# Kernel optimization log

Measured on AMD Instinct MI355X. Metric: run time of the kernel, lower is better.

The kernel has to match this reference:

```python
import jax, jax.numpy as jnp
import numpy as np

B, S, H = 2, 2048, 1024
NH, HD = 16, 64  # num heads, head dim
EPS = 1e-12


def setup_inputs() -> dict:
    key = jax.random.key(0)
    ks = jax.random.split(key, 10)
    scale = 0.02
    return {
        "hidden_states": jax.random.normal(ks[0], (B, S, H), jnp.float32),
        "attention_mask": jnp.zeros((B, 1, 1, S), jnp.float32),
        "Wq": jax.random.normal(ks[1], (H, H), jnp.float32) * scale,
        "bq": jnp.zeros((H,), jnp.float32),
        "Wk": jax.random.normal(ks[2], (H, H), jnp.float32) * scale,
        "bk": jnp.zeros((H,), jnp.float32),
        "Wv": jax.random.normal(ks[3], (H, H), jnp.float32) * scale,
        "bv": jnp.zeros((H,), jnp.float32),
        "Wo": jax.random.normal(ks[4], (H, H), jnp.float32) * scale,
        "bo": jnp.zeros((H,), jnp.float32),
        "ln_gamma": jnp.ones((H,), jnp.float32),
        "ln_beta": jnp.zeros((H,), jnp.float32),
    }


def _split_heads(x):
    # [B,S,H] -> [B,NH,S,HD]
    b, s, _ = x.shape
    return x.reshape(b, s, NH, HD).transpose(0, 2, 1, 3)


def reference(hidden_states, attention_mask, Wq, bq, Wk, bk, Wv, bv, Wo, bo, ln_gamma, ln_beta):
    q = _split_heads(hidden_states @ Wq + bq)
    k = _split_heads(hidden_states @ Wk + bk)
    v = _split_heads(hidden_states @ Wv + bv)

    # unfused SDPA, as in source: matmul -> scale -> mask -> softmax -> matmul
    scores = jnp.einsum('bhqd,bhkd->bhqk', q, k) / jnp.sqrt(jnp.float32(HD))
    scores = scores + attention_mask
    probs = jax.nn.softmax(scores, axis=-1)  # dropout p=0 (eval)
    ctx = jnp.einsum('bhqk,bhkd->bhqd', probs, v)
    ctx = ctx.transpose(0, 2, 1, 3).reshape(hidden_states.shape)  # [B,S,H]

    # BaseBertSelfOutput: dense -> (dropout p=0) -> LayerNorm(residual)
    out = ctx @ Wo + bo
    res = out + hidden_states
    mu = jnp.mean(res, axis=-1, keepdims=True)
    var = jnp.mean(jnp.square(res - mu), axis=-1, keepdims=True)
    normed = (res - mu) * jax.lax.rsqrt(var + EPS)
    return normed * ln_gamma + ln_beta
```

## Files before the change

kernel.cpp:

```cpp
#include <hip/hip_runtime.h>
#include <hip/hip_bf16.h>

#define B_  2
#define S_  2048
#define H_  1024
#define NH_ 16
#define HD_ 64
#define EPSLN 1e-12f

typedef short bf16x8 __attribute__((ext_vector_type(8)));
typedef float f32x4  __attribute__((ext_vector_type(4)));

__device__ __forceinline__ float bf2f(ushort u) {
    union { unsigned int i; float f; } v; v.i = ((unsigned int)u) << 16; return v.f;
}
__device__ __forceinline__ ushort f2bf(float f) {
    union { float f; unsigned int i; } v; v.f = f;
    unsigned int r = v.i + 0x7FFFu + ((v.i >> 16) & 1u);
    return (ushort)(r >> 16);
}
__device__ __forceinline__ ushort f2bf_hw(float f) {
    __hip_bfloat16 h = __float2bfloat16(f);
    return *reinterpret_cast<ushort*>(&h);
}
__device__ __forceinline__ unsigned int pack_bf2(float a, float b) {
    return ((unsigned int)f2bf_hw(b) << 16) | (unsigned int)f2bf_hw(a);
}

__global__ __launch_bounds__(256) void cvt_f32_bf16(const float* __restrict__ in,
                                                    ushort* __restrict__ out, int n) {
    int i = (blockIdx.x * 256 + threadIdx.x) * 4;
    float4 v = *(const float4*)&in[i];
    ushort4 o = make_ushort4(f2bf(v.x), f2bf(v.y), f2bf(v.z), f2bf(v.w));
    *(ushort4*)&out[i] = o;
}

__global__ __launch_bounds__(256) void transpose_cvt(
        const float* __restrict__ W0, const float* __restrict__ W1,
        const float* __restrict__ W2, const float* __restrict__ W3,
        ushort* __restrict__ T0, ushort* __restrict__ T1,
        ushort* __restrict__ T2, ushort* __restrict__ T3) {
    const int z = blockIdx.z;
    const float* in = (z == 0) ? W0 : (z == 1) ? W1 : (z == 2) ? W2 : W3;
    ushort* out     = (z == 0) ? T0 : (z == 1) ? T1 : (z == 2) ? T2 : T3;

    __shared__ float tile[64][65];
    const int bx = blockIdx.x * 64, by = blockIdx.y * 64;
    const int t = threadIdx.x;
    #pragma unroll
    for (int i = 0; i < 16; i++) {
        int idx = t + i * 256;
        int r = idx >> 6, c = idx & 63;
        tile[r][c] = in[(by + r) * 1024 + bx + c];
    }
    __syncthreads();
    #pragma unroll
    for (int i = 0; i < 16; i++) {
        int idx = t + i * 256;
        int r = idx >> 6, c = idx & 63;
        out[(bx + r) * 1024 + by + c] = f2bf(tile[c][r]);
    }
}

__global__ __launch_bounds__(256) void v_transpose(const ushort* __restrict__ Vb,
                                                   ushort* __restrict__ VtG) {
    __shared__ ushort tile[64][72];
    const int s0 = blockIdx.x * 64;
    const int head = blockIdx.y;
    const ushort* src = Vb + (size_t)head * S_ * HD_;
    ushort* dst       = VtG + (size_t)head * S_ * HD_;
    const int t = threadIdx.x, lane = t & 63, w = t >> 6;

    uint4 a = *(const uint4*)&src[(s0 + lane) * HD_ + w * 16];
    uint4 b = *(const uint4*)&src[(s0 + lane) * HD_ + w * 16 + 8];
    const ushort* pa = (const ushort*)&a;
    #pragma unroll
    for (int i = 0; i < 8; i++) tile[w * 16 + i][lane] = pa[i];
    const ushort* pb = (const ushort*)&b;
    #pragma unroll
    for (int i = 0; i < 8; i++) tile[w * 16 + 8 + i][lane] = pb[i];
    __syncthreads();

    const int d = t >> 2, sc = (t & 3) * 16;
    uint4 o1 = *(const uint4*)&tile[d][sc];
    uint4 o2 = *(const uint4*)&tile[d][sc + 8];
    *(uint4*)&dst[d * S_ + s0 + sc]     = o1;
    *(uint4*)&dst[d * S_ + s0 + sc + 8] = o2;
}

__global__ __launch_bounds__(256) void qkv_gemm(
        const ushort* __restrict__ X,
        const ushort* __restrict__ Wqt, const ushort* __restrict__ Wkt, const ushort* __restrict__ Wvt,
        const float* __restrict__ bq,  const float* __restrict__ bk,  const float* __restrict__ bv,
        ushort* __restrict__ Qo, ushort* __restrict__ Ko, ushort* __restrict__ Vo) {
    const int which = blockIdx.z;
    const ushort* Wt  = (which == 0) ? Wqt : (which == 1) ? Wkt : Wvt;
    const float* bias = (which == 0) ? bq  : (which == 1) ? bk  : bv;
    ushort* Out       = (which == 0) ? Qo  : (which == 1) ? Ko  : Vo;

    __shared__ ushort As[128][72];
    __shared__ ushort Bs[128][72];
    const int m0 = blockIdx.x * 128, n0 = blockIdx.y * 128;
    const int t = threadIdx.x;
    const int lane = t & 63, w = t >> 6;
    const int wr = (w >> 1) * 64, wc = (w & 1) * 64;
    const int l15 = lane & 15, l4 = lane >> 4;

    f32x4 acc[4][4] = {};
    const int sr = t >> 3, sc = (t & 7) * 8;

    for (int k0 = 0; k0 < H_; k0 += 64) {
        __syncthreads();
        #pragma unroll
        for (int p = 0; p < 4; p++) {
            uint4 av  = *(const uint4*)&X [(m0 + p * 32 + sr) * H_ + k0 + sc];
            uint4 bv2 = *(const uint4*)&Wt[(n0 + p * 32 + sr) * H_ + k0 + sc];
            *(uint4*)&As[p * 32 + sr][sc] = av;
            *(uint4*)&Bs[p * 32 + sr][sc] = bv2;
        }
        __syncthreads();
        #pragma unroll
        for (int ks = 0; ks < 2; ks++) {
            bf16x8 af[4], bfr[4];
            #pragma unroll
            for (int i = 0; i < 4; i++) af[i]  = *(const bf16x8*)&As[wr + i * 16 + l15][ks * 32 + l4 * 8];
            #pragma unroll
            for (int i = 0; i < 4; i++) bfr[i] = *(const bf16x8*)&Bs[wc + i * 16 + l15][ks * 32 + l4 * 8];
            #pragma unroll
            for (int mi = 0; mi < 4; mi++)
                #pragma unroll
                for (int ni = 0; ni < 4; ni++)
                    acc[mi][ni] = __builtin_amdgcn_mfma_f32_16x16x32_bf16(af[mi], bfr[ni], acc[mi][ni], 0, 0, 0);
        }
    }

    #pragma unroll
    for (int ni = 0; ni < 4; ni++) {
        int n = n0 + wc + ni * 16 + l15;
        float bvf = bias[n];
        int h = n >> 6, d = n & 63;
        #pragma unroll
        for (int mi = 0; mi < 4; mi++) {
            int mrow = m0 + wr + mi * 16 + l4 * 4;
            #pragma unroll
            for (int j = 0; j < 4; j++) {
                int m = mrow + j;
                int b = m >> 11, s = m & 2047;
                Out[((b * NH_ + h) * S_ + s) * HD_ + d] = f2bf(acc[mi][ni][j] + bvf);
            }
        }
    }
}

__global__ __launch_bounds__(256) void flash_attn(
        const ushort* __restrict__ Q, const ushort* __restrict__ K, const ushort* __restrict__ VtG,
        const float* __restrict__ mask, ushort* __restrict__ ctx) {
    __shared__ __align__(16) ushort Ks[64][72];
    __shared__ __align__(16) ushort Vt[64][72];
    __shared__ __align__(16) ushort Ps[4][16][72];

    const int qt = blockIdx.x, h = blockIdx.y, b = blockIdx.z;
    const int t = threadIdx.x, lane = t & 63, w = t >> 6;
    const int l15 = lane & 15, l4 = lane >> 4;
    const size_t head_off = ((size_t)(b * NH_ + h)) * S_ * HD_;
    const ushort* Qh = Q + head_off;
    const ushort* Kh = K + head_off;
    const ushort* Vh = VtG + head_off;

    const int qrow = qt * 64 + w * 16 + l15;
    bf16x8 qf[2];
    qf[0] = *(const bf16x8*)&Qh[qrow * 64 + 0  + l4 * 8];
    qf[1] = *(const bf16x8*)&Qh[qrow * 64 + 32 + l4 * 8];

    f32x4 ctx_acc[4] = {};
    float mrun = -1e30f, lrun = 0.f;

    const int sr = t >> 2, sc0 = (t & 3) * 8;
    const int vd = t >> 2, vsc = (t & 3) * 16;

    for (int kv0 = 0; kv0 < S_; kv0 += 64) {
        __syncthreads();
        {
            uint4 k1 = *(const uint4*)&Kh[(kv0 + sr) * 64 + sc0];
            uint4 k2 = *(const uint4*)&Kh[(kv0 + sr) * 64 + sc0 + 32];
            uint4 v1 = *(const uint4*)&Vh[vd * S_ + kv0 + vsc];
            uint4 v2 = *(const uint4*)&Vh[vd * S_ + kv0 + vsc + 8];
            *(uint4*)&Ks[sr][sc0]      = k1;
            *(uint4*)&Ks[sr][sc0 + 32] = k2;
            *(uint4*)&Vt[vd][vsc]      = v1;
            *(uint4*)&Vt[vd][vsc + 8]  = v2;
        }
        __syncthreads();

        f32x4 sacc[4] = {};
        #pragma unroll
        for (int ks = 0; ks < 2; ks++) {
            bf16x8 kf[4];
            #pragma unroll
            for (int n = 0; n < 4; n++) kf[n] = *(const bf16x8*)&Ks[n * 16 + l15][ks * 32 + l4 * 8];
            #pragma unroll
            for (int n = 0; n < 4; n++)
                sacc[n] = __builtin_amdgcn_mfma_f32_16x16x32_bf16(kf[n], qf[ks], sacc[n], 0, 0, 0);
        }

        float tmax = -1e30f;
        #pragma unroll
        for (int n = 0; n < 4; n++) {
            float4 mk4 = *(const float4*)&mask[b * S_ + kv0 + n * 16 + l4 * 4];
            sacc[n][0] = sacc[n][0] * 0.125f + mk4.x;
            sacc[n][1] = sacc[n][1] * 0.125f + mk4.y;
            sacc[n][2] = sacc[n][2] * 0.125f + mk4.z;
            sacc[n][3] = sacc[n][3] * 0.125f + mk4.w;
            tmax = fmaxf(tmax, fmaxf(fmaxf(sacc[n][0], sacc[n][1]), fmaxf(sacc[n][2], sacc[n][3])));
        }
        tmax = fmaxf(tmax, __shfl_xor(tmax, 16, 64));
        tmax = fmaxf(tmax, __shfl_xor(tmax, 32, 64));

        float mnew = fmaxf(mrun, tmax);
        float scale = __expf(mrun - mnew);
        mrun = mnew;

        float tsum = 0.f;
        #pragma unroll
        for (int n = 0; n < 4; n++) {
            float p0 = __expf(sacc[n][0] - mnew);
            float p1 = __expf(sacc[n][1] - mnew);
            float p2 = __expf(sacc[n][2] - mnew);
            float p3 = __expf(sacc[n][3] - mnew);
            tsum += (p0 + p1) + (p2 + p3);
            uint2 pw = make_uint2(pack_bf2(p0, p1), pack_bf2(p2, p3));
            *(uint2*)&Ps[w][l15][n * 16 + l4 * 4] = pw;
        }
        tsum += __shfl_xor(tsum, 16, 64);
        tsum += __shfl_xor(tsum, 32, 64);
        lrun = lrun * scale + tsum;

        float sj[4];
        #pragma unroll
        for (int j = 0; j < 4; j++) sj[j] = __shfl(scale, l4 * 4 + j, 64);
        #pragma unroll
        for (int df = 0; df < 4; df++)
            #pragma unroll
            for (int j = 0; j < 4; j++) ctx_acc[df][j] *= sj[j];

        #pragma unroll
        for (int ks = 0; ks < 2; ks++) {
            bf16x8 pf = *(const bf16x8*)&Ps[w][l15][ks * 32 + l4 * 8];
            #pragma unroll
            for (int df = 0; df < 4; df++) {
                bf16x8 vf = *(const bf16x8*)&Vt[df * 16 + l15][ks * 32 + l4 * 8];
                ctx_acc[df] = __builtin_amdgcn_mfma_f32_16x16x32_bf16(pf, vf, ctx_acc[df], 0, 0, 0);
            }
        }
    }

    float lr[4];
    #pragma unroll
    for (int j = 0; j < 4; j++) lr[j] = 1.0f / __shfl(lrun, l4 * 4 + j, 64);
    #pragma unroll
    for (int df = 0; df < 4; df++) {
        int col = h * HD_ + df * 16 + l15;
        #pragma unroll
        for (int j = 0; j < 4; j++) {
            int s = qt * 64 + w * 16 + l4 * 4 + j;
            ctx[((size_t)b * S_ + s) * H_ + col] = f2bf(ctx_acc[df][j] * lr[j]);
        }
    }
}

__global__ __launch_bounds__(256) void out_proj(
        const ushort* __restrict__ Ctx, const ushort* __restrict__ Wot,
        const float* __restrict__ bo,  const float* __restrict__ Hs,
        float* __restrict__ Tmp) {
    __shared__ ushort As[128][72];
    __shared__ ushort Bs[128][72];
    const int m0 = blockIdx.x * 128, n0 = blockIdx.y * 128;
    const int t = threadIdx.x;
    const int lane = t & 63, w = t >> 6;
    const int wr = (w >> 1) * 64, wc = (w & 1) * 64;
    const int l15 = lane & 15, l4 = lane >> 4;

    f32x4 acc[4][4] = {};
    const int sr = t >> 3, sc = (t & 7) * 8;

    for (int k0 = 0; k0 < H_; k0 += 64) {
        __syncthreads();
        #pragma unroll
        for (int p = 0; p < 4; p++) {
            uint4 av  = *(const uint4*)&Ctx[(m0 + p * 32 + sr) * H_ + k0 + sc];
            uint4 bv2 = *(const uint4*)&Wot[(n0 + p * 32 + sr) * H_ + k0 + sc];
            *(uint4*)&As[p * 32 + sr][sc] = av;
            *(uint4*)&Bs[p * 32 + sr][sc] = bv2;
        }
        __syncthreads();
        #pragma unroll
        for (int ks = 0; ks < 2; ks++) {
            bf16x8 af[4], bfr[4];
            #pragma unroll
            for (int i = 0; i < 4; i++) af[i]  = *(const bf16x8*)&As[wr + i * 16 + l15][ks * 32 + l4 * 8];
            #pragma unroll
            for (int i = 0; i < 4; i++) bfr[i] = *(const bf16x8*)&Bs[wc + i * 16 + l15][ks * 32 + l4 * 8];
            #pragma unroll
            for (int mi = 0; mi < 4; mi++)
                #pragma unroll
                for (int ni = 0; ni < 4; ni++)
                    acc[mi][ni] = __builtin_amdgcn_mfma_f32_16x16x32_bf16(af[mi], bfr[ni], acc[mi][ni], 0, 0, 0);
        }
    }

    #pragma unroll
    for (int ni = 0; ni < 4; ni++) {
        int n = n0 + wc + ni * 16 + l15;
        float bvf = bo[n];
        #pragma unroll
        for (int mi = 0; mi < 4; mi++) {
            int mrow = m0 + wr + mi * 16 + l4 * 4;
            #pragma unroll
            for (int j = 0; j < 4; j++) {
                int m = mrow + j;
                Tmp[(size_t)m * H_ + n] = acc[mi][ni][j] + bvf + Hs[(size_t)m * H_ + n];
            }
        }
    }
}

__global__ __launch_bounds__(256) void ln_kernel(
        const float* __restrict__ Tmp, const float* __restrict__ gamma,
        const float* __restrict__ beta, float* __restrict__ Out) {
    const int row = blockIdx.x;
    const float* x = Tmp + (size_t)row * H_;
    const int t = threadIdx.x, w = t >> 6, lane = t & 63;

    float4 v = *(const float4*)&x[t * 4];
    float s = v.x + v.y + v.z + v.w;
    #pragma unroll
    for (int m = 1; m < 64; m <<= 1) s += __shfl_xor(s, m, 64);
    __shared__ float red[4], red2[4];
    if (lane == 0) red[w] = s;
    __syncthreads();
    float mu = (red[0] + red[1] + red[2] + red[3]) * (1.0f / H_);

    float d0 = v.x - mu, d1 = v.y - mu, d2 = v.z - mu, d3 = v.w - mu;
    float sq = d0 * d0 + d1 * d1 + d2 * d2 + d3 * d3;
    #pragma unroll
    for (int m = 1; m < 64; m <<= 1) sq += __shfl_xor(sq, m, 64);
    if (lane == 0) red2[w] = sq;
    __syncthreads();
    float var = (red2[0] + red2[1] + red2[2] + red2[3]) * (1.0f / H_);
    float rstd = rsqrtf(var + EPSLN);

    float dd[4] = {d0, d1, d2, d3};
    float4 o;
    o.x = dd[0] * rstd * gamma[t * 4 + 0] + beta[t * 4 + 0];
    o.y = dd[1] * rstd * gamma[t * 4 + 1] + beta[t * 4 + 1];
    o.z = dd[2] * rstd * gamma[t * 4 + 2] + beta[t * 4 + 2];
    o.w = dd[3] * rstd * gamma[t * 4 + 3] + beta[t * 4 + 3];
    *(float4*)&Out[(size_t)row * H_ + t * 4] = o;
}

extern "C" void kernel_launch(void* const* d_in, const int* in_sizes, int n_in,
                              void* d_out, int out_size, void* d_ws, size_t ws_size,
                              hipStream_t stream) {
    const float* hs    = (const float*)d_in[0];
    const float* mask  = (const float*)d_in[1];
    const float* Wq    = (const float*)d_in[2];
    const float* bq    = (const float*)d_in[3];
    const float* Wk    = (const float*)d_in[4];
    const float* bk    = (const float*)d_in[5];
    const float* Wv    = (const float*)d_in[6];
    const float* bv    = (const float*)d_in[7];
    const float* Wo    = (const float*)d_in[8];
    const float* bo    = (const float*)d_in[9];
    const float* gamma = (const float*)d_in[10];
    const float* beta  = (const float*)d_in[11];

    char* ws = (char*)d_ws;
    const size_t WSZ = (size_t)H_ * H_;
    const size_t TSZ = (size_t)B_ * S_ * H_;
    ushort* Wqt = (ushort*)ws;
    ushort* Wkt = Wqt + WSZ;
    ushort* Wvt = Wkt + WSZ;
    ushort* Wot = Wvt + WSZ;
    ushort* Xb  = Wot + WSZ;
    ushort* Qb  = Xb + TSZ;
    ushort* Kb  = Qb + TSZ;
    ushort* Vb  = Kb + TSZ;
    ushort* Ctx = Vb + TSZ;
    float*  Tmp = (float*)(Ctx + TSZ);
    ushort* VtG = (ushort*)Tmp;

    cvt_f32_bf16<<<TSZ / (256 * 4), 256, 0, stream>>>(hs, Xb, (int)TSZ);
    transpose_cvt<<<dim3(16, 16, 4), 256, 0, stream>>>(Wq, Wk, Wv, Wo, Wqt, Wkt, Wvt, Wot);

    qkv_gemm<<<dim3(32, 8, 3), 256, 0, stream>>>(Xb, Wqt, Wkt, Wvt, bq, bk, bv, Qb, Kb, Vb);
    v_transpose<<<dim3(S_ / 64, B_ * NH_), 256, 0, stream>>>(Vb, VtG);
    flash_attn<<<dim3(32, 16, 2), 256, 0, stream>>>(Qb, Kb, VtG, mask, Ctx);
    out_proj<<<dim3(32, 8), 256, 0, stream>>>(Ctx, Wot, bo, hs, Tmp);
    ln_kernel<<<B_ * S_, 256, 0, stream>>>(Tmp, gamma, beta, (float*)d_out);
}
```

Before: 168.4 us.

## Prefetch K/V tiles, use exp2 softmax, and remap attention blocks per XCD

The flash attention loop now holds the next K/V tile in registers, loaded while the current tile is consumed, so global load latency overlaps with compute. Softmax switches to exp2 by folding log2(e) into the score scale, with a new small kernel that pre-scales the mask into scratch space reused from the bf16 input buffer. The attention grid is flattened and remapped so consecutive blocks on each XCD share the same head, aiming for better L2 reuse of K/V. The trade-offs are an extra kernel launch, more registers per thread, and reliance on the bf16 input buffer being dead once the QKV GEMM has run.

After: 176.0 us. 4.5% more time.

```diff
diff --git a/kernel.cpp b/kernel.cpp
--- a/kernel.cpp
+++ b/kernel.cpp
@@ -7,6 +7,7 @@
 #define NH_ 16
 #define HD_ 64
 #define EPSLN 1e-12f
+#define LOG2E 1.4426950408889634f
 
 typedef short bf16x8 __attribute__((ext_vector_type(8)));
 typedef float f32x4  __attribute__((ext_vector_type(4)));
@@ -33,6 +34,12 @@
     float4 v = *(const float4*)&in[i];
     ushort4 o = make_ushort4(f2bf(v.x), f2bf(v.y), f2bf(v.z), f2bf(v.w));
     *(ushort4*)&out[i] = o;
+}
+
+__global__ __launch_bounds__(256) void scale_mask(const float* __restrict__ in,
+                                                  float* __restrict__ out) {
+    int i = blockIdx.x * 256 + threadIdx.x;
+    out[i] = in[i] * LOG2E;
 }
 
 __global__ __launch_bounds__(256) void transpose_cvt(
@@ -154,15 +161,20 @@
 
 __global__ __launch_bounds__(256) void flash_attn(
         const ushort* __restrict__ Q, const ushort* __restrict__ K, const ushort* __restrict__ VtG,
-        const float* __restrict__ mask, ushort* __restrict__ ctx) {
+        const float* __restrict__ maskL2, ushort* __restrict__ ctx) {
     __shared__ __align__(16) ushort Ks[64][72];
     __shared__ __align__(16) ushort Vt[64][72];
     __shared__ __align__(16) ushort Ps[4][16][72];
 
-    const int qt = blockIdx.x, h = blockIdx.y, b = blockIdx.z;
+    const int wgid = blockIdx.x;
+    const int vid  = (wgid & 7) * 128 + (wgid >> 3);
+    const int qt   = vid & 31;
+    const int hb   = vid >> 5;
+    const int h    = hb & (NH_ - 1), b = hb >> 4;
+
     const int t = threadIdx.x, lane = t & 63, w = t >> 6;
     const int l15 = lane & 15, l4 = lane >> 4;
-    const size_t head_off = ((size_t)(b * NH_ + h)) * S_ * HD_;
+    const size_t head_off = (size_t)hb * S_ * HD_;
     const ushort* Qh = Q + head_off;
     const ushort* Kh = K + head_off;
     const ushort* Vh = VtG + head_off;
@@ -175,20 +187,27 @@
     f32x4 ctx_acc[4] = {};
     float mrun = -1e30f, lrun = 0.f;
 
-    const int sr = t >> 2, sc0 = (t & 3) * 8;
-    const int vd = t >> 2, vsc = (t & 3) * 16;
+    const int sr  = t >> 2, sc0 = (t & 3) * 8;
+    const int vsc = (t & 3) * 16;
+
+    uint4 kr0 = *(const uint4*)&Kh[sr * 64 + sc0];
+    uint4 kr1 = *(const uint4*)&Kh[sr * 64 + sc0 + 32];
+    uint4 vr0 = *(const uint4*)&Vh[sr * S_ + vsc];
+    uint4 vr1 = *(const uint4*)&Vh[sr * S_ + vsc + 8];
+
+    const float ksc = 0.125f * LOG2E;
 
     for (int kv0 = 0; kv0 < S_; kv0 += 64) {
         __syncthreads();
-        {
-            uint4 k1 = *(const uint4*)&Kh[(kv0 + sr) * 64 + sc0];
-            uint4 k2 = *(const uint4*)&Kh[(kv0 + sr) * 64 + sc0 + 32];
-            uint4 v1 = *(const uint4*)&Vh[vd * S_ + kv0 + vsc];
-            uint4 v2 = *(const uint4*)&Vh[vd * S_ + kv0 + vsc + 8];
-            *(uint4*)&Ks[sr][sc0]      = k1;
-            *(uint4*)&Ks[sr][sc0 + 32] = k2;
-            *(uint4*)&Vt[vd][vsc]      = v1;
-            *(uint4*)&Vt[vd][vsc + 8]  = v2;
+        *(uint4*)&Ks[sr][sc0]      = kr0;
+        *(uint4*)&Ks[sr][sc0 + 32] = kr1;
+        *(uint4*)&Vt[sr][vsc]      = vr0;
+        *(uint4*)&Vt[sr][vsc + 8]  = vr1;
+        if (kv0 + 64 < S_) {
+            kr0 = *(const uint4*)&Kh[(kv0 + 64 + sr) * 64 + sc0];
+            kr1 = *(const uint4*)&Kh[(kv0 + 64 + sr) * 64 + sc0 + 32];
+            vr0 = *(const uint4*)&Vh[sr * S_ + kv0 + 64 + vsc];
+            vr1 = *(const uint4*)&Vh[sr * S_ + kv0 + 64 + vsc + 8];
         }
         __syncthreads();
 
@@ -206,27 +225,27 @@
         float tmax = -1e30f;
         #pragma unroll
         for (int n = 0; n < 4; n++) {
-            float4 mk4 = *(const float4*)&mask[b * S_ + kv0 + n * 16 + l4 * 4];
-            sacc[n][0] = sacc[n][0] * 0.125f + mk4.x;
-            sacc[n][1] = sacc[n][1] * 0.125f + mk4.y;
-            sacc[n][2] = sacc[n][2] * 0.125f + mk4.z;
-            sacc[n][3] = sacc[n][3] * 0.125f + mk4.w;
+            float4 mk4 = *(const float4*)&maskL2[b * S_ + kv0 + n * 16 + l4 * 4];
+            sacc[n][0] = fmaf(sacc[n][0], ksc, mk4.x);
+            sacc[n][1] = fmaf(sacc[n][1], ksc, mk4.y);
+            sacc[n][2] = fmaf(sacc[n][2], ksc, mk4.z);
+            sacc[n][3] = fmaf(sacc[n][3], ksc, mk4.w);
             tmax = fmaxf(tmax, fmaxf(fmaxf(sacc[n][0], sacc[n][1]), fmaxf(sacc[n][2], sacc[n][3])));
         }
         tmax = fmaxf(tmax, __shfl_xor(tmax, 16, 64));
         tmax = fmaxf(tmax, __shfl_xor(tmax, 32, 64));
 
-        float mnew = fmaxf(mrun, tmax);
-        float scale = __expf(mrun - mnew);
+        float mnew  = fmaxf(mrun, tmax);
+        float scale = exp2f(mrun - mnew);
         mrun = mnew;
 
         float tsum = 0.f;
         #pragma unroll
         for (int n = 0; n < 4; n++) {
-            float p0 = __expf(sacc[n][0] - mnew);
-            float p1 = __expf(sacc[n][1] - mnew);
-            float p2 = __expf(sacc[n][2] - mnew);
-            float p3 = __expf(sacc[n][3] - mnew);
+            float p0 = exp2f(sacc[n][0] - mnew);
+            float p1 = exp2f(sacc[n][1] - mnew);
+            float p2 = exp2f(sacc[n][2] - mnew);
+            float p3 = exp2f(sacc[n][3] - mnew);
             tsum += (p0 + p1) + (p2 + p3);
             uint2 pw = make_uint2(pack_bf2(p0, p1), pack_bf2(p2, p3));
             *(uint2*)&Ps[w][l15][n * 16 + l4 * 4] = pw;
@@ -388,13 +407,15 @@
     ushort* Ctx = Vb + TSZ;
     float*  Tmp = (float*)(Ctx + TSZ);
     ushort* VtG = (ushort*)Tmp;
+    float* MaskL2 = (float*)Xb;
 
     cvt_f32_bf16<<<TSZ / (256 * 4), 256, 0, stream>>>(hs, Xb, (int)TSZ);
     transpose_cvt<<<dim3(16, 16, 4), 256, 0, stream>>>(Wq, Wk, Wv, Wo, Wqt, Wkt, Wvt, Wot);
 
     qkv_gemm<<<dim3(32, 8, 3), 256, 0, stream>>>(Xb, Wqt, Wkt, Wvt, bq, bk, bv, Qb, Kb, Vb);
+    scale_mask<<<(B_ * S_) / 256, 256, 0, stream>>>(mask, MaskL2);
     v_transpose<<<dim3(S_ / 64, B_ * NH_), 256, 0, stream>>>(Vb, VtG);
-    flash_attn<<<dim3(32, 16, 2), 256, 0, stream>>>(Qb, Kb, VtG, mask, Ctx);
+    flash_attn<<<dim3(1024), 256, 0, stream>>>(Qb, Kb, VtG, MaskL2, Ctx);
     out_proj<<<dim3(32, 8), 256, 0, stream>>>(Ctx, Wot, bo, hs, Tmp);
     ln_kernel<<<B_ * S_, 256, 0, stream>>>(Tmp, gamma, beta, (float*)d_out);
 }
```
